# Kernel tuning notes

Measured on AMD Instinct MI355X. Metric: run time of the kernel, lower is better.

Reference implementation:

```python
import jax, jax.numpy as jnp
import numpy as np

# Static configuration (from init_kwargs)
B, T, SP = 4, 100, 20          # batch, max_time_patches, max_space_patches
S = T * SP                      # flattened seq len = 2000
H, NH = 512, 8                  # hidden size, heads
D = H // NH                     # head dim = 64
CF, CB = 4, 4                   # context_forward, context_backward
ROPE_BASE = 10000.0
NEG = -1e9


def setup_inputs() -> dict:
    key = jax.random.key(0)
    ks = jax.random.split(key, 8)
    w = 1.0 / np.sqrt(H)
    x = jax.random.normal(ks[0], (B, S, H), jnp.float32)
    # token order is space-major: timestamps = time-patch id repeated per space patch
    timestamps = jnp.broadcast_to(jnp.tile(jnp.arange(T, dtype=jnp.int32), SP), (B, S))
    attn_mask = jnp.ones((B, S), jnp.int32)
    Wq = jax.random.normal(ks[1], (H, H), jnp.float32) * w
    Wk = jax.random.normal(ks[2], (H, H), jnp.float32) * w
    Wv = jax.random.normal(ks[3], (H, H), jnp.float32) * w
    Wo = jax.random.normal(ks[4], (H, H), jnp.float32) * w
    z = jnp.zeros((H,), jnp.float32)
    return {"x": x, "attn_mask": attn_mask, "timestamps": timestamps,
            "Wq": Wq, "bq": z, "Wk": Wk, "bk": z, "Wv": Wv, "bv": z,
            "Wo": Wo, "bo": z}


def _rotate_half(u):
    return jnp.concatenate((-u[..., D // 2:], u[..., :D // 2]), axis=-1)


def _rope_tables():
    inv_freq = 1.0 / (ROPE_BASE ** (jnp.arange(0, D, 2, dtype=jnp.float32) / D))
    t = jnp.arange(T, dtype=jnp.float32)
    freqs = t[:, None] * inv_freq[None, :]          # [T, D/2]
    emb = jnp.concatenate((freqs, freqs), axis=-1)  # [T, D]
    return jnp.cos(emb), jnp.sin(emb)


def _context_mask():
    # forward/backward banded window in time, tiled over space patches
    ones = jnp.ones((T, T), jnp.float32)
    m = jnp.triu(ones, k=-CF).T          # allow up to CF future time patches
    if CB > 0:
        m = m * jnp.triu(ones, k=-CB)    # allow up to CB past time patches
    return jnp.tile(m, (SP, SP))         # [S, S]


def reference(x, attn_mask, timestamps, Wq, bq, Wk, bk, Wv, bv, Wo, bo):
    # projections -> [B, NH, S, D]
    def heads(w, b):
        return (x @ w + b).reshape(B, S, NH, D).transpose(0, 2, 1, 3)
    q, k, v = heads(Wq, bq), heads(Wk, bk), heads(Wv, bv)

    # rotary position embedding indexed by time-patch timestamps
    cos_t, sin_t = _rope_tables()
    cos = cos_t[timestamps][:, None]     # [B, 1, S, D]
    sin = sin_t[timestamps][:, None]
    q = q * cos + _rotate_half(q) * sin
    k = k * cos + _rotate_half(k) * sin

    # banded-context masked attention
    scores = jnp.einsum('bhqd,bhkd->bhqk', q, k) / jnp.sqrt(jnp.float32(D))
    mask = (_context_mask()[None, None, :, :] *
            attn_mask[:, None, None, :].astype(jnp.float32)) > 0
    scores = jnp.where(mask, scores, NEG)
    attn = jax.nn.softmax(scores, axis=-1)
    out = jnp.einsum('bhqk,bhkd->bhqd', attn, v)
    out = out.transpose(0, 2, 1, 3).reshape(B, S, H)
    return out @ Wo + bo
```

## Files before the change

### kernel.cpp

```cpp
#include <hip/hip_runtime.h>
#include <hip/hip_bf16.h>
#include <stdint.h>


typedef __bf16 bf16x8 __attribute__((ext_vector_type(8)));
typedef float f32x4 __attribute__((ext_vector_type(4)));

static const size_t O_XB = 0;
static const size_t O_WT = 8192000;
static const size_t O_Q  = 10289152;
static const size_t O_K  = 18481152;
static const size_t O_V  = 26673152;
static const size_t O_RC = 34865152;
static const size_t O_RS = 34877952;
static const size_t O_VT = 34890752;

__device__ inline void gload16(const void* g, void* l) {
  __builtin_amdgcn_global_load_lds((const __attribute__((address_space(1))) void*)g,
                                   (__attribute__((address_space(3))) void*)l, 16, 0, 0);
}

__global__ __launch_bounds__(256) void prep_kernel(
    const float* __restrict__ x, const float* __restrict__ Wq, const float* __restrict__ Wk,
    const float* __restrict__ Wv, const float* __restrict__ Wo,
    __bf16* __restrict__ xb, __bf16* __restrict__ wt,
    float* __restrict__ ropeC, float* __restrict__ ropeS)
{
  const int tid = blockIdx.x * 256 + threadIdx.x;
  if (tid < 1024000) {
    float4 v = ((const float4*)x)[tid];
    union { ushort4 u; __bf16 b[4]; } p;
    p.b[0] = (__bf16)v.x; p.b[1] = (__bf16)v.y; p.b[2] = (__bf16)v.z; p.b[3] = (__bf16)v.w;
    ((ushort4*)xb)[tid] = p.u;
  }
  {
    const int mat = tid >> 18;
    const int r = tid & 262143;
    const int n = r >> 9, k = r & 511;
    const float* W = (mat == 0) ? Wq : (mat == 1) ? Wk : (mat == 2) ? Wv : Wo;
    wt[(size_t)mat * 262144 + n * 512 + k] = (__bf16)W[k * 512 + n];
  }
  if (tid < 3200) {
    const int t = tid >> 5, i = tid & 31;
    const float f = (float)t * powf(10000.0f, -(float)i / 32.0f);
    ropeC[tid] = cosf(f);
    ropeS[tid] = sinf(f);
  }
}

__device__ inline void gemm_core(const __bf16* __restrict__ A, const __bf16* __restrict__ Bm,
                                 __bf16* As, __bf16* Bs, f32x4 (&acc)[4][4],
                                 int m0, int n0, int tid, int wm, int wn, int lr, int g)
{
  const int r0 = tid >> 2;
  const int aq = tid & 3;
  for (int kk = 0; kk < 512; kk += 32) {
    int gm0 = m0 + r0;      if (gm0 > 7999) gm0 = 7999;
    int gm1 = m0 + r0 + 64; if (gm1 > 7999) gm1 = 7999;
    gload16(A + (size_t)gm0 * 512 + kk + aq * 8, As + tid * 8);
    gload16(A + (size_t)gm1 * 512 + kk + aq * 8, As + tid * 8 + 2048);
    gload16(Bm + (size_t)(n0 + r0) * 512 + kk + aq * 8, Bs + tid * 8);
    gload16(Bm + (size_t)(n0 + r0 + 64) * 512 + kk + aq * 8, Bs + tid * 8 + 2048);
    asm volatile("s_waitcnt vmcnt(0)" ::: "memory");
    __syncthreads();
    bf16x8 af[4], bfr[4];
#pragma unroll
    for (int f = 0; f < 4; ++f) {
      af[f]  = *(const bf16x8*)(As + (wm + f * 16 + lr) * 32 + g * 8);
      bfr[f] = *(const bf16x8*)(Bs + (wn + f * 16 + lr) * 32 + g * 8);
    }
#pragma unroll
    for (int i = 0; i < 4; ++i) {
#pragma unroll
      for (int j = 0; j < 4; ++j)
        acc[i][j] = __builtin_amdgcn_mfma_f32_16x16x32_bf16(af[i], bfr[j], acc[i][j], 0, 0, 0);
    }
    __syncthreads();
  }
}

__global__ __launch_bounds__(256) void qkv_gemm(
    const __bf16* __restrict__ xb, const __bf16* __restrict__ wt,
    const float* __restrict__ bq, const float* __restrict__ bk, const float* __restrict__ bv,
    const float* __restrict__ ropeC, const float* __restrict__ ropeS,
    __bf16* __restrict__ qws, __bf16* __restrict__ kws, __bf16* __restrict__ vws)
{
  const int tid = threadIdx.x;
  const int m0 = blockIdx.x * 128, n0 = blockIdx.y * 128;
  const int mat = blockIdx.z;
  __shared__ __bf16 As[4096], Bs[4096];
  f32x4 acc[4][4] = {};
  const int wid = tid >> 6, lane = tid & 63;
  const int wm = (wid >> 1) << 6, wn = (wid & 1) << 6;
  const int lr = lane & 15, g = lane >> 4;

  gemm_core(xb, wt + (size_t)mat * 262144, As, Bs, acc, m0, n0, tid, wm, wn, lr, g);

  const int hn = (n0 + wn) >> 6;
  const float* bias = (mat == 0) ? bq : (mat == 1) ? bk : bv;
  __bf16* outp = (mat == 0) ? qws : (mat == 1) ? kws : vws;
  const float qscale = (mat == 0) ? 0.125f : 1.0f;

#pragma unroll
  for (int i = 0; i < 4; ++i) {
#pragma unroll
    for (int r = 0; r < 4; ++r) {
      const int m = m0 + wm + i * 16 + g * 4 + r;
      if (m >= 8000) continue;
      const int b = m / 2000;
      const int s = m - b * 2000;
      const int t = s % 100;
      const int sp = s / 100;
      const int pos = t * 20 + sp;
      const size_t ob = ((size_t)(b * 8 + hn) * 2000 + pos) * 64;
      if (mat == 2) {
#pragma unroll
        for (int j = 0; j < 4; ++j) {
          float v = acc[i][j][r] + bias[n0 + wn + j * 16 + lr];
          outp[ob + j * 16 + lr] = (__bf16)v;
        }
      } else {
#pragma unroll
        for (int j = 0; j < 2; ++j) {
          const int dlo = j * 16 + lr;
          const float alo = acc[i][j][r]     + bias[n0 + wn + j * 16 + lr];
          const float ahi = acc[i][j + 2][r] + bias[n0 + wn + (j + 2) * 16 + lr];
          const float cs = ropeC[t * 32 + dlo], sn = ropeS[t * 32 + dlo];
          const float olo = (alo * cs - ahi * sn) * qscale;
          const float ohi = (ahi * cs + alo * sn) * qscale;
          outp[ob + dlo]      = (__bf16)olo;
          outp[ob + dlo + 32] = (__bf16)ohi;
        }
      }
    }
  }
}

__global__ __launch_bounds__(256) void vt_transpose(
    const __bf16* __restrict__ v, __bf16* __restrict__ vt)
{
  __shared__ __align__(16) __bf16 tile[64][68];
  const int tid = threadIdx.x;
  const int p0 = blockIdx.x * 64;
  const int bh = blockIdx.y;
  const __bf16* vp = v + (size_t)bh * 2000 * 64;
  __bf16* vtp = vt + (size_t)bh * 64 * 2000;
  const int np = (p0 + 64 <= 2000) ? 64 : (2000 - p0);

#pragma unroll
  for (int it = 0; it < 4; ++it) {
    const int idx = it * 256 + tid;
    const int pl = idx >> 4, d4 = (idx & 15) * 4;
    if (pl < np) {
      const ushort4 u = *(const ushort4*)(vp + (size_t)(p0 + pl) * 64 + d4);
      *(ushort4*)&tile[pl][d4] = u;
    }
  }
  __syncthreads();
#pragma unroll
  for (int it = 0; it < 16; ++it) {
    const int idx = it * 256 + tid;
    const int d = idx >> 6, p = idx & 63;
    if (p < np) vtp[(size_t)d * 2000 + p0 + p] = tile[p][d];
  }
}

__global__ __launch_bounds__(256) void attn_kernel(
    const __bf16* __restrict__ qw, const __bf16* __restrict__ kw, const __bf16* __restrict__ vt,
    const int* __restrict__ amask, __bf16* __restrict__ aout)
{
  const int wid = threadIdx.x >> 6, lane = threadIdx.x & 63;
  const int lr = lane & 15, g = lane >> 4;
  const int tq = blockIdx.x * 4 + wid;
  const int h = blockIdx.y, b = blockIdx.z;

  int t0 = tq - 4; if (t0 < 0) t0 = 0;
  int t1 = tq + 4; if (t1 > 99) t1 = 99;
  const int k0 = t0 * 20;
  const int nk = (t1 - t0 + 1) * 20;
  const int base = k0 & ~7;

  __shared__ __bf16 Pl[4][20][200];
  __shared__ float addm[4][192];

  const size_t hb = (size_t)(b * 8 + h) * 2000;
  const __bf16* qp = qw + (hb + (size_t)tq * 20) * 64;
  const __bf16* vtp = vt + (size_t)(b * 8 + h) * 64 * 2000;

  for (int k = lane; k < 192; k += 64) {
    const int kg = base + k;
    float v = -1e9f;
    if (kg >= k0 && kg < k0 + nk) {
      const int tk = kg / 20;
      const int spk = kg - tk * 20;
      if (amask[b * 2000 + spk * 100 + tk] != 0) v = 0.0f;
    }
    addm[wid][k] = v;
  }

  bf16x8 qf[2][2];
#pragma unroll
  for (int jq = 0; jq < 2; ++jq) {
    int q = jq * 16 + lr; if (q > 19) q = 19;
#pragma unroll
    for (int ks = 0; ks < 2; ++ks)
      qf[jq][ks] = *(const bf16x8*)(qp + q * 64 + ks * 32 + g * 8);
  }

  f32x4 acc[12][2] = {};
#pragma unroll
  for (int i = 0; i < 12; ++i) {
    int krow = base + i * 16 + lr; if (krow > 1999) krow = 1999;
    const __bf16* kr = kw + (hb + (size_t)krow) * 64;
    const bf16x8 af0 = *(const bf16x8*)(kr + g * 8);
    const bf16x8 af1 = *(const bf16x8*)(kr + 32 + g * 8);
    acc[i][0] = __builtin_amdgcn_mfma_f32_16x16x32_bf16(af0, qf[0][0], acc[i][0], 0, 0, 0);
    acc[i][0] = __builtin_amdgcn_mfma_f32_16x16x32_bf16(af1, qf[0][1], acc[i][0], 0, 0, 0);
    acc[i][1] = __builtin_amdgcn_mfma_f32_16x16x32_bf16(af0, qf[1][0], acc[i][1], 0, 0, 0);
    acc[i][1] = __builtin_amdgcn_mfma_f32_16x16x32_bf16(af1, qf[1][1], acc[i][1], 0, 0, 0);
  }

  __syncthreads();

#pragma unroll
  for (int jq = 0; jq < 2; ++jq) {
    float mx = -1e30f;
#pragma unroll
    for (int i = 0; i < 12; ++i)
#pragma unroll
      for (int r = 0; r < 4; ++r) {
        acc[i][jq][r] += addm[wid][i * 16 + g * 4 + r];
        mx = fmaxf(mx, acc[i][jq][r]);
      }
    mx = fmaxf(mx, __shfl_xor(mx, 16));
    mx = fmaxf(mx, __shfl_xor(mx, 32));
    float sm = 0.0f;
#pragma unroll
    for (int i = 0; i < 12; ++i)
#pragma unroll
      for (int r = 0; r < 4; ++r) {
        const float p = __expf(acc[i][jq][r] - mx);
        acc[i][jq][r] = p;
        sm += p;
      }
    sm += __shfl_xor(sm, 16);
    sm += __shfl_xor(sm, 32);
    const float rinv = 1.0f / sm;
    const int q = jq * 16 + lr;
    if (q < 20) {
#pragma unroll
      for (int i = 0; i < 12; ++i) {
        union { ushort4 u; __bf16 e[4]; } pk;
        pk.e[0] = (__bf16)(acc[i][jq][0] * rinv);
        pk.e[1] = (__bf16)(acc[i][jq][1] * rinv);
        pk.e[2] = (__bf16)(acc[i][jq][2] * rinv);
        pk.e[3] = (__bf16)(acc[i][jq][3] * rinv);
        *(ushort4*)&Pl[wid][q][i * 16 + g * 4] = pk.u;
      }
    }
  }

  __syncthreads();

  f32x4 acc2[2][4] = {};
#pragma unroll
  for (int kb = 0; kb < 6; ++kb) {
    int kv = base + kb * 32 + g * 8; if (kv >= 2000) kv = 0;
    bf16x8 bfv[4];
#pragma unroll
    for (int j2 = 0; j2 < 4; ++j2)
      bfv[j2] = *(const bf16x8*)(vtp + (size_t)(j2 * 16 + lr) * 2000 + kv);
#pragma unroll
    for (int i2 = 0; i2 < 2; ++i2) {
      int qr = i2 * 16 + lr; if (qr > 19) qr = 19;
      const bf16x8 pa = *(const bf16x8*)&Pl[wid][qr][kb * 32 + g * 8];
#pragma unroll
      for (int j2 = 0; j2 < 4; ++j2)
        acc2[i2][j2] = __builtin_amdgcn_mfma_f32_16x16x32_bf16(pa, bfv[j2], acc2[i2][j2], 0, 0, 0);
    }
  }

#pragma unroll
  for (int i2 = 0; i2 < 2; ++i2)
#pragma unroll
    for (int r = 0; r < 4; ++r) {
      const int q = i2 * 16 + g * 4 + r;
      if (q < 20) {
        const size_t ob = ((size_t)b * 2000 + q * 100 + tq) * 512 + h * 64;
#pragma unroll
        for (int j2 = 0; j2 < 4; ++j2)
          aout[ob + j2 * 16 + lr] = (__bf16)acc2[i2][j2][r];
      }
    }
}

__global__ __launch_bounds__(256) void out_gemm(
    const __bf16* __restrict__ ab, const __bf16* __restrict__ wot,
    const float* __restrict__ bo, float* __restrict__ out)
{
  const int tid = threadIdx.x;
  const int m0 = blockIdx.x * 128, n0 = blockIdx.y * 128;
  __shared__ __bf16 As[4096], Bs[4096];
  f32x4 acc[4][4] = {};
  const int wid = tid >> 6, lane = tid & 63;
  const int wm = (wid >> 1) << 6, wn = (wid & 1) << 6;
  const int lr = lane & 15, g = lane >> 4;

  gemm_core(ab, wot, As, Bs, acc, m0, n0, tid, wm, wn, lr, g);

#pragma unroll
  for (int i = 0; i < 4; ++i) {
#pragma unroll
    for (int r = 0; r < 4; ++r) {
      const int m = m0 + wm + i * 16 + g * 4 + r;
      if (m < 8000) {
#pragma unroll
        for (int j = 0; j < 4; ++j) {
          const int n = n0 + wn + j * 16 + lr;
          out[(size_t)m * 512 + n] = acc[i][j][r] + bo[n];
        }
      }
    }
  }
}

extern "C" void kernel_launch(void* const* d_in, const int* in_sizes, int n_in,
                              void* d_out, int out_size, void* d_ws, size_t ws_size,
                              hipStream_t stream) {
  const float* x   = (const float*)d_in[0];
  const int* amask = (const int*)d_in[1];
  const float* Wq = (const float*)d_in[3];
  const float* bq = (const float*)d_in[4];
  const float* Wk = (const float*)d_in[5];
  const float* bk = (const float*)d_in[6];
  const float* Wv = (const float*)d_in[7];
  const float* bv = (const float*)d_in[8];
  const float* Wo = (const float*)d_in[9];
  const float* bo = (const float*)d_in[10];
  float* out = (float*)d_out;

  char* ws = (char*)d_ws;
  __bf16* xb    = (__bf16*)(ws + O_XB);
  __bf16* wt    = (__bf16*)(ws + O_WT);
  __bf16* qws   = (__bf16*)(ws + O_Q);
  __bf16* kws   = (__bf16*)(ws + O_K);
  __bf16* vws   = (__bf16*)(ws + O_V);
  float*  ropeC = (float*)(ws + O_RC);
  float*  ropeS = (float*)(ws + O_RS);
  __bf16* vtw   = (__bf16*)(ws + O_VT);
  __bf16* aout  = (__bf16*)(ws + O_XB);

  prep_kernel<<<4096, 256, 0, stream>>>(x, Wq, Wk, Wv, Wo, xb, wt, ropeC, ropeS);
  qkv_gemm<<<dim3(63, 4, 3), 256, 0, stream>>>(xb, wt, bq, bk, bv, ropeC, ropeS, qws, kws, vws);
  vt_transpose<<<dim3(32, 32), 256, 0, stream>>>(vws, vtw);
  attn_kernel<<<dim3(25, 8, 4), 256, 0, stream>>>(qws, kws, vtw, amask, aout);
  out_gemm<<<dim3(63, 4, 1), 256, 0, stream>>>(aout, wt + 3 * 262144, bo, out);
}
```

Baseline: 91.10 us.

## Double-buffer GEMM LDS loads, XCD-swizzle GEMM grids, tile weight transpose, set MFMA priority

The GEMM core now double-buffers its LDS tiles, so the global loads for the next k-step are issued before the MFMAs on the current one, which is meant to hide load latency. The QKV and output GEMMs switch to a 1D grid remapped per XCD so that neighbouring tiles share L2. The weight transpose in the prep kernel goes through a shared-memory tile to get coalesced reads and writes. The attention MFMA loops raise wave priority with s_setprio. Doubling LDS use per block may reduce occupancy.

```diff
diff --git a/kernel.cpp b/kernel.cpp
--- a/kernel.cpp
+++ b/kernel.cpp
@@ -20,62 +20,100 @@
                                    (__attribute__((address_space(3))) void*)l, 16, 0, 0);
 }
 
+__device__ inline int xcd_swz(int orig, int nwg) {
+  const int q8 = nwg >> 3, r8 = nwg & 7;
+  const int xcd = orig & 7;
+  return (xcd < r8 ? xcd * (q8 + 1) : r8 * (q8 + 1) + (xcd - r8) * q8) + (orig >> 3);
+}
+
 __global__ __launch_bounds__(256) void prep_kernel(
     const float* __restrict__ x, const float* __restrict__ Wq, const float* __restrict__ Wk,
     const float* __restrict__ Wv, const float* __restrict__ Wo,
     __bf16* __restrict__ xb, __bf16* __restrict__ wt,
     float* __restrict__ ropeC, float* __restrict__ ropeS)
 {
-  const int tid = blockIdx.x * 256 + threadIdx.x;
-  if (tid < 1024000) {
-    float4 v = ((const float4*)x)[tid];
+  __shared__ float tile[64][65];
+  const int tid = threadIdx.x;
+  const int bx = blockIdx.x;
+  if (bx < 4000) {
+    const int idx = bx * 256 + tid;
+    float4 v = ((const float4*)x)[idx];
     union { ushort4 u; __bf16 b[4]; } p;
     p.b[0] = (__bf16)v.x; p.b[1] = (__bf16)v.y; p.b[2] = (__bf16)v.z; p.b[3] = (__bf16)v.w;
-    ((ushort4*)xb)[tid] = p.u;
-  }
-  {
-    const int mat = tid >> 18;
-    const int r = tid & 262143;
-    const int n = r >> 9, k = r & 511;
-    const float* W = (mat == 0) ? Wq : (mat == 1) ? Wk : (mat == 2) ? Wv : Wo;
-    wt[(size_t)mat * 262144 + n * 512 + k] = (__bf16)W[k * 512 + n];
-  }
-  if (tid < 3200) {
-    const int t = tid >> 5, i = tid & 31;
-    const float f = (float)t * powf(10000.0f, -(float)i / 32.0f);
-    ropeC[tid] = cosf(f);
-    ropeS[tid] = sinf(f);
-  }
-}
-
-__device__ inline void gemm_core(const __bf16* __restrict__ A, const __bf16* __restrict__ Bm,
-                                 __bf16* As, __bf16* Bs, f32x4 (&acc)[4][4],
-                                 int m0, int n0, int tid, int wm, int wn, int lr, int g)
+    ((ushort4*)xb)[idx] = p.u;
+    return;
+  }
+  const int wb = bx - 4000;
+  const int mat = wb >> 6, sub = wb & 63;
+  const int tk = (sub >> 3) * 64, tn = (sub & 7) * 64;
+  const float* W = (mat == 0) ? Wq : (mat == 1) ? Wk : (mat == 2) ? Wv : Wo;
+#pragma unroll
+  for (int it = 0; it < 16; ++it) {
+    const int idx = it * 256 + tid;
+    const int kl = idx >> 6, nl = idx & 63;
+    tile[kl][nl] = W[(size_t)(tk + kl) * 512 + tn + nl];
+  }
+  __syncthreads();
+#pragma unroll
+  for (int it = 0; it < 16; ++it) {
+    const int idx = it * 256 + tid;
+    const int nl = idx >> 6, kl = idx & 63;
+    wt[(size_t)mat * 262144 + (size_t)(tn + nl) * 512 + tk + kl] = (__bf16)tile[kl][nl];
+  }
+  if (wb == 0) {
+    for (int idx = tid; idx < 3200; idx += 256) {
+      const int t = idx >> 5, i = idx & 31;
+      const float f = (float)t * powf(10000.0f, -(float)i / 32.0f);
+      ropeC[idx] = cosf(f);
+      ropeS[idx] = sinf(f);
+    }
+  }
+}
+
+__device__ inline void gemm_core_db(const __bf16* __restrict__ A, const __bf16* __restrict__ Bm,
+                                    __bf16* As, __bf16* Bs, f32x4 (&acc)[4][4],
+                                    int m0, int n0, int tid, int wm, int wn, int lr, int g)
 {
   const int r0 = tid >> 2;
   const int aq = tid & 3;
+  int gm0 = m0 + r0;      if (gm0 > 7999) gm0 = 7999;
+  int gm1 = m0 + r0 + 64; if (gm1 > 7999) gm1 = 7999;
+  const __bf16* a0 = A + (size_t)gm0 * 512 + aq * 8;
+  const __bf16* a1 = A + (size_t)gm1 * 512 + aq * 8;
+  const __bf16* b0 = Bm + (size_t)(n0 + r0) * 512 + aq * 8;
+  const __bf16* b1 = Bm + (size_t)(n0 + r0 + 64) * 512 + aq * 8;
+
+  gload16(a0, As + tid * 8);
+  gload16(a1, As + tid * 8 + 2048);
+  gload16(b0, Bs + tid * 8);
+  gload16(b1, Bs + tid * 8 + 2048);
+  asm volatile("s_waitcnt vmcnt(0)" ::: "memory");
+  __syncthreads();
+
+  int cur = 0;
   for (int kk = 0; kk < 512; kk += 32) {
-    int gm0 = m0 + r0;      if (gm0 > 7999) gm0 = 7999;
-    int gm1 = m0 + r0 + 64; if (gm1 > 7999) gm1 = 7999;
-    gload16(A + (size_t)gm0 * 512 + kk + aq * 8, As + tid * 8);
-    gload16(A + (size_t)gm1 * 512 + kk + aq * 8, As + tid * 8 + 2048);
-    gload16(Bm + (size_t)(n0 + r0) * 512 + kk + aq * 8, Bs + tid * 8);
-    gload16(Bm + (size_t)(n0 + r0 + 64) * 512 + kk + aq * 8, Bs + tid * 8 + 2048);
-    asm volatile("s_waitcnt vmcnt(0)" ::: "memory");
-    __syncthreads();
+    const int nxt = cur ^ 1;
+    if (kk + 32 < 512) {
+      gload16(a0 + kk + 32, As + nxt * 4096 + tid * 8);
+      gload16(a1 + kk + 32, As + nxt * 4096 + tid * 8 + 2048);
+      gload16(b0 + kk + 32, Bs + nxt * 4096 + tid * 8);
+      gload16(b1 + kk + 32, Bs + nxt * 4096 + tid * 8 + 2048);
+    }
     bf16x8 af[4], bfr[4];
 #pragma unroll
     for (int f = 0; f < 4; ++f) {
-      af[f]  = *(const bf16x8*)(As + (wm + f * 16 + lr) * 32 + g * 8);
-      bfr[f] = *(const bf16x8*)(Bs + (wn + f * 16 + lr) * 32 + g * 8);
-    }
-#pragma unroll
-    for (int i = 0; i < 4; ++i) {
+      af[f]  = *(const bf16x8*)(As + cur * 4096 + (wm + f * 16 + lr) * 32 + g * 8);
+      bfr[f] = *(const bf16x8*)(Bs + cur * 4096 + (wn + f * 16 + lr) * 32 + g * 8);
+    }
+#pragma unroll
+    for (int i = 0; i < 4; ++i)
 #pragma unroll
       for (int j = 0; j < 4; ++j)
         acc[i][j] = __builtin_amdgcn_mfma_f32_16x16x32_bf16(af[i], bfr[j], acc[i][j], 0, 0, 0);
-    }
+    if (kk + 32 < 512)
+      asm volatile("s_waitcnt vmcnt(0)" ::: "memory");
     __syncthreads();
+    cur = nxt;
   }
 }
 
@@ -86,15 +124,19 @@
     __bf16* __restrict__ qws, __bf16* __restrict__ kws, __bf16* __restrict__ vws)
 {
   const int tid = threadIdx.x;
-  const int m0 = blockIdx.x * 128, n0 = blockIdx.y * 128;
-  const int mat = blockIdx.z;
-  __shared__ __bf16 As[4096], Bs[4096];
+  const int wgid = xcd_swz(blockIdx.x, 756);
+  const int mt = wgid / 12;
+  const int rest = wgid - mt * 12;
+  const int mat = rest >> 2;
+  const int nt = rest & 3;
+  const int m0 = mt * 128, n0 = nt * 128;
+  __shared__ __bf16 As[8192], Bs[8192];
   f32x4 acc[4][4] = {};
   const int wid = tid >> 6, lane = tid & 63;
   const int wm = (wid >> 1) << 6, wn = (wid & 1) << 6;
   const int lr = lane & 15, g = lane >> 4;
 
-  gemm_core(xb, wt + (size_t)mat * 262144, As, Bs, acc, m0, n0, tid, wm, wn, lr, g);
+  gemm_core_db(xb, wt + (size_t)mat * 262144, As, Bs, acc, m0, n0, tid, wm, wn, lr, g);
 
   const int hn = (n0 + wn) >> 6;
   const float* bias = (mat == 0) ? bq : (mat == 1) ? bk : bv;
@@ -208,6 +250,7 @@
   }
 
   f32x4 acc[12][2] = {};
+  __builtin_amdgcn_s_setprio(1);
 #pragma unroll
   for (int i = 0; i < 12; ++i) {
     int krow = base + i * 16 + lr; if (krow > 1999) krow = 1999;
@@ -219,6 +262,7 @@
     acc[i][1] = __builtin_amdgcn_mfma_f32_16x16x32_bf16(af0, qf[1][0], acc[i][1], 0, 0, 0);
     acc[i][1] = __builtin_amdgcn_mfma_f32_16x16x32_bf16(af1, qf[1][1], acc[i][1], 0, 0, 0);
   }
+  __builtin_amdgcn_s_setprio(0);
 
   __syncthreads();
 
@@ -263,6 +307,7 @@
   __syncthreads();
 
   f32x4 acc2[2][4] = {};
+  __builtin_amdgcn_s_setprio(1);
 #pragma unroll
   for (int kb = 0; kb < 6; ++kb) {
     int kv = base + kb * 32 + g * 8; if (kv >= 2000) kv = 0;
@@ -279,6 +324,7 @@
         acc2[i2][j2] = __builtin_amdgcn_mfma_f32_16x16x32_bf16(pa, bfv[j2], acc2[i2][j2], 0, 0, 0);
     }
   }
+  __builtin_amdgcn_s_setprio(0);
 
 #pragma unroll
   for (int i2 = 0; i2 < 2; ++i2)
@@ -299,14 +345,16 @@
     const float* __restrict__ bo, float* __restrict__ out)
 {
   const int tid = threadIdx.x;
-  const int m0 = blockIdx.x * 128, n0 = blockIdx.y * 128;
-  __shared__ __bf16 As[4096], Bs[4096];
+  const int wgid = xcd_swz(blockIdx.x, 252);
+  const int mt = wgid >> 2, nt = wgid & 3;
+  const int m0 = mt * 128, n0 = nt * 128;
+  __shared__ __bf16 As[8192], Bs[8192];
   f32x4 acc[4][4] = {};
   const int wid = tid >> 6, lane = tid & 63;
   const int wm = (wid >> 1) << 6, wn = (wid & 1) << 6;
   const int lr = lane & 15, g = lane >> 4;
 
-  gemm_core(ab, wot, As, Bs, acc, m0, n0, tid, wm, wn, lr, g);
+  gemm_core_db(ab, wot, As, Bs, acc, m0, n0, tid, wm, wn, lr, g);
 
 #pragma unroll
   for (int i = 0; i < 4; ++i) {
@@ -350,9 +398,9 @@
   __bf16* vtw   = (__bf16*)(ws + O_VT);
   __bf16* aout  = (__bf16*)(ws + O_XB);
 
-  prep_kernel<<<4096, 256, 0, stream>>>(x, Wq, Wk, Wv, Wo, xb, wt, ropeC, ropeS);
-  qkv_gemm<<<dim3(63, 4, 3), 256, 0, stream>>>(xb, wt, bq, bk, bv, ropeC, ropeS, qws, kws, vws);
+  prep_kernel<<<4256, 256, 0, stream>>>(x, Wq, Wk, Wv, Wo, xb, wt, ropeC, ropeS);
+  qkv_gemm<<<756, 256, 0, stream>>>(xb, wt, bq, bk, bv, ropeC, ropeS, qws, kws, vws);
   vt_transpose<<<dim3(32, 32), 256, 0, stream>>>(vws, vtw);
   attn_kernel<<<dim3(25, 8, 4), 256, 0, stream>>>(qws, kws, vtw, amask, aout);
-  out_gemm<<<dim3(63, 4, 1), 256, 0, stream>>>(aout, wt + 3 * 262144, bo, out);
-}
+  out_gemm<<<252, 256, 0, stream>>>(aout, wt + 3 * 262144, bo, out);
+}
```

Result: no change. 89.55 us (-1.7%).
